# Optimization experiments

Hardware: AMD Instinct MI355X
Metric: run time of the kernel (lower is better)

The kernel has to match this reference:

```python
import jax, jax.numpy as jnp
import numpy as np

N, D, H = 4096, 1024, 16
GAMMA = 1.0


def setup_inputs() -> dict:
    key = jax.random.key(0)
    ks = jax.random.split(key, 10)
    s = 1.0 / np.sqrt(D)
    return {
        "x": jax.random.normal(ks[0], (N, D), jnp.float32),
        "h": jax.random.normal(ks[1], (N,), jnp.float32),
        "Wq": jax.random.normal(ks[2], (D, D), jnp.float32) * s,
        "bq": jax.random.normal(ks[3], (D,), jnp.float32) * s,
        "Wk": jax.random.normal(ks[4], (D, D), jnp.float32) * s,
        "bk": jax.random.normal(ks[5], (D,), jnp.float32) * s,
        "Wv": jax.random.normal(ks[6], (D, D), jnp.float32) * s,
        "bv": jax.random.normal(ks[7], (D,), jnp.float32) * s,
        "Wo": jax.random.normal(ks[8], (D, D), jnp.float32) * s,
        "bo": jax.random.normal(ks[9], (D,), jnp.float32) * s,
    }


def reference(x, h, Wq, bq, Wk, bk, Wv, bv, Wo, bo):
    n, d = x.shape
    d_head = d // H
    # torch Linear: y = x @ W.T + b
    q = (x @ Wq.T + bq).reshape(n, H, d_head)
    k = (x @ Wk.T + bk).reshape(n, H, d_head)
    v = (x @ Wv.T + bv).reshape(n, H, d_head)
    scale = 1.0 / np.sqrt(d_head).astype(np.float32)
    logits = jnp.einsum('nhd,mhd->hnm', q, k) * scale  # (H, n, n)
    logits = logits - (GAMMA * h)[None, None, :]       # per-key additive bias
    attn = jax.nn.softmax(logits, axis=-1)
    out = jnp.einsum('hnm,mhd->nhd', attn, v).reshape(n, d)
    return out @ Wo.T + bo + x
```

## Files before the change

kernel.cpp:

```cpp
#include <hip/hip_runtime.h>
#include <hip/hip_bf16.h>
#include <stdint.h>

#define NTOK 4096
#define DM   1024
#define NH   16
#define DH   64
#define SCL  0.1803368801111129f
#define LOG2E 1.4426950408889634f

typedef __attribute__((ext_vector_type(8)))  short bf16x8;
typedef __attribute__((ext_vector_type(4)))  float f32x4;
typedef __attribute__((ext_vector_type(16))) float f32x16;
typedef __attribute__((ext_vector_type(4)))  unsigned short us4;

__device__ inline unsigned short f2bf(float f) {
  union { float f; unsigned int u; } a;
  a.f = f;
  unsigned int u = a.u;
  u += 0x7fffu + ((u >> 16) & 1u);
  return (unsigned short)(u >> 16);
}

__device__ inline unsigned int cvtpk_bf16(float lo, float hi) {
  unsigned int r;
  asm("v_cvt_pk_bf16_f32 %0, %1, %2" : "=v"(r) : "v"(lo), "v"(hi));
  return r;
}

__device__ inline void gload_lds16(const void* gsrc, void* ldst) {
  __builtin_amdgcn_global_load_lds(
      (const __attribute__((address_space(1))) void*)(uintptr_t)gsrc,
      (__attribute__((address_space(3))) void*)(unsigned int)(uintptr_t)ldst,
      16, 0, 0);
}

__global__ void cvt_fused(const float* __restrict__ x,
                          const float* __restrict__ Wq,
                          const float* __restrict__ Wk,
                          const float* __restrict__ Wv,
                          const float* __restrict__ Wo,
                          const float* __restrict__ h,
                          unsigned short* __restrict__ xb,
                          unsigned short* __restrict__ wqkvb,
                          unsigned short* __restrict__ wob,
                          float* __restrict__ hperm) {
  const int b = blockIdx.x;
  if (b >= 8192) {
    int i = (b - 8192) * 256 + threadIdx.x;
    int r  = i & 15;
    int hh = (i >> 4) & 1;
    int t  = i >> 5;
    int key = t * 32 + (r & 3) + 8 * (r >> 2) + 4 * hh;
    hperm[i] = -LOG2E * h[key];
    return;
  }
  int i = b * 256 + threadIdx.x;
  const float* src; unsigned short* dst; int off;
  if (i < 1048576)      { src = x;  dst = xb;                 off = i; }
  else if (i < 1310720) { src = Wq; dst = wqkvb;              off = i - 1048576; }
  else if (i < 1572864) { src = Wk; dst = wqkvb + DM * DM;    off = i - 1310720; }
  else if (i < 1835008) { src = Wv; dst = wqkvb + 2 * DM * DM; off = i - 1572864; }
  else                  { src = Wo; dst = wob;                off = i - 1835008; }
  float4 v = ((const float4*)src)[off];
  us4 o;
  o[0] = f2bf(v.x); o[1] = f2bf(v.y); o[2] = f2bf(v.z); o[3] = f2bf(v.w);
  ((us4*)dst)[off] = o;
}

__global__ __launch_bounds__(256)
void gemm_qkv(const unsigned short* __restrict__ A,
              const unsigned short* __restrict__ B,
              const float* __restrict__ bq, const float* __restrict__ bk,
              const float* __restrict__ bv,
              unsigned short* __restrict__ Qb, unsigned short* __restrict__ Kb,
              unsigned short* __restrict__ Vt)
{
  const int bid = blockIdx.x;
  const int wg  = (bid & 7) * 96 + (bid >> 3);
  const int bn  = (wg % 24) * 128;
  const int bm  = (wg / 24) * 128;
  const int tid  = threadIdx.x;
  const int wid  = tid >> 6;
  const int lane = tid & 63;
  const int wr = wid >> 1;
  const int wc = wid & 1;

  __shared__ __align__(16) unsigned short As[128 * 32];
  __shared__ __align__(16) unsigned short Bs[128 * 32];

  f32x4 acc[4][4];
#pragma unroll
  for (int i = 0; i < 4; i++)
#pragma unroll
    for (int j = 0; j < 4; j++) acc[i][j] = f32x4{0.f, 0.f, 0.f, 0.f};

  const int fr = lane & 15;
  const int fk = (lane >> 4) * 8;
  const int srow = lane >> 2;
  const int scol = (lane & 3) * 8;

  for (int k0 = 0; k0 < DM; k0 += 32) {
#pragma unroll
    for (int c = 0; c < 2; ++c) {
      const int chunk = wid * 2 + c;
      gload_lds16(A + (size_t)(bm + chunk * 16 + srow) * DM + k0 + scol,
                  &As[chunk * 512]);
      gload_lds16(B + (size_t)(bn + chunk * 16 + srow) * DM + k0 + scol,
                  &Bs[chunk * 512]);
    }
    __syncthreads();
    bf16x8 af[4], bfr[4];
#pragma unroll
    for (int i = 0; i < 4; i++)
      af[i] = *(const bf16x8*)&As[(wr * 64 + i * 16 + fr) * 32 + fk];
#pragma unroll
    for (int j = 0; j < 4; j++)
      bfr[j] = *(const bf16x8*)&Bs[(wc * 64 + j * 16 + fr) * 32 + fk];
#pragma unroll
    for (int i = 0; i < 4; i++)
#pragma unroll
      for (int j = 0; j < 4; j++)
        acc[i][j] = __builtin_amdgcn_mfma_f32_16x16x32_bf16(af[i], bfr[j],
                                                            acc[i][j], 0, 0, 0);
    __syncthreads();
  }

  const int fq = lane >> 4;
  const int region = bn >> 10;
  const float* bias = (region == 0) ? bq : (region == 1) ? bk : bv;
  const float qscale = (region == 0) ? SCL : 1.0f;
  unsigned short* outp = (region == 0) ? Qb : Kb;
#pragma unroll
  for (int j = 0; j < 4; j++) {
    const int col = bn + wc * 64 + j * 16 + fr;
    const int cl  = col & 1023;
    const float bvx = bias[cl];
#pragma unroll
    for (int i = 0; i < 4; i++) {
      const int row0 = bm + wr * 64 + i * 16 + fq * 4;
      if (region < 2) {
#pragma unroll
        for (int r = 0; r < 4; r++)
          outp[(size_t)(row0 + r) * DM + cl] = f2bf((acc[i][j][r] + bvx) * qscale);
      } else {
        us4 pk;
#pragma unroll
        for (int r = 0; r < 4; r++) pk[r] = f2bf(acc[i][j][r] + bvx);
        *(us4*)&Vt[(size_t)cl * NTOK + row0] = pk;
      }
    }
  }
}

__global__ __launch_bounds__(256)
void gemm_out(const unsigned short* __restrict__ A,
              const unsigned short* __restrict__ B,
              const float* __restrict__ bias,
              const float* __restrict__ resid,
              float* __restrict__ Cf)
{
  const int bid = blockIdx.x;
  const int wg  = (bid & 7) * 64 + (bid >> 3);
  const int bn  = (wg % 16) * 64;
  const int bm  = (wg / 16) * 128;
  const int tid  = threadIdx.x;
  const int wid  = tid >> 6;
  const int lane = tid & 63;

  __shared__ __align__(16) unsigned short As[128 * 32];
  __shared__ __align__(16) unsigned short Bs[64 * 32];

  f32x4 acc[2][4];
#pragma unroll
  for (int i = 0; i < 2; i++)
#pragma unroll
    for (int j = 0; j < 4; j++) acc[i][j] = f32x4{0.f, 0.f, 0.f, 0.f};

  const int fr = lane & 15;
  const int fk = (lane >> 4) * 8;
  const int srow = lane >> 2;
  const int scol = (lane & 3) * 8;

  for (int k0 = 0; k0 < DM; k0 += 32) {
#pragma unroll
    for (int c = 0; c < 3; ++c) {
      const int chunk = wid * 3 + c;
      if (chunk < 8) {
        gload_lds16(A + (size_t)(bm + chunk * 16 + srow) * DM + k0 + scol,
                    &As[chunk * 512]);
      } else {
        gload_lds16(B + (size_t)(bn + (chunk - 8) * 16 + srow) * DM + k0 + scol,
                    &Bs[(chunk - 8) * 512]);
      }
    }
    __syncthreads();
    bf16x8 af[2], bfr[4];
#pragma unroll
    for (int i = 0; i < 2; i++)
      af[i] = *(const bf16x8*)&As[(wid * 32 + i * 16 + fr) * 32 + fk];
#pragma unroll
    for (int j = 0; j < 4; j++)
      bfr[j] = *(const bf16x8*)&Bs[(j * 16 + fr) * 32 + fk];
#pragma unroll
    for (int i = 0; i < 2; i++)
#pragma unroll
      for (int j = 0; j < 4; j++)
        acc[i][j] = __builtin_amdgcn_mfma_f32_16x16x32_bf16(af[i], bfr[j],
                                                            acc[i][j], 0, 0, 0);
    __syncthreads();
  }

  const int fq = lane >> 4;
#pragma unroll
  for (int j = 0; j < 4; j++) {
    const int col = bn + j * 16 + fr;
    const float bvx = bias[col];
#pragma unroll
    for (int i = 0; i < 2; i++) {
      const int row0 = bm + wid * 32 + i * 16 + fq * 4;
#pragma unroll
      for (int r = 0; r < 4; r++) {
        const size_t idx = (size_t)(row0 + r) * DM + col;
        Cf[idx] = acc[i][j][r] + bvx + resid[idx];
      }
    }
  }
}

#define MFMA32(a, b, c) __builtin_amdgcn_mfma_f32_32x32x16_bf16(a, b, c, 0, 0, 0)

__global__ __launch_bounds__(512)
void attn_kernel(const unsigned short* __restrict__ Q,
                 const unsigned short* __restrict__ K,
                 const unsigned short* __restrict__ Vt,
                 const float* __restrict__ hperm,
                 unsigned short* __restrict__ O)
{
  const int wgid = (blockIdx.x & 7) * 64 + (blockIdx.x >> 3);
  const int head = wgid >> 5;
  const int qblk = wgid & 31;
  const int tid  = threadIdx.x;
  const int wid  = tid >> 6;
  const int grp  = wid >> 2;
  const int w4   = wid & 3;
  const int lane = tid & 63;
  const int c31  = lane & 31;
  const int hi   = lane >> 5;
  const int qwb  = qblk * 128 + w4 * 32;
  const int k0g  = grp * 2048;

  __shared__ __align__(16) char lds_raw[32768];
  char* kbase = lds_raw + grp * 16384;
  char* vbase = kbase + 8192;

  const int srow = w4 * 4 + (lane >> 4);
  const int ssl  = lane & 15;
  const int kq   = ssl ^ srow;
  const int kkey = srow + 16 * (kq >> 3);
  const unsigned short* kg =
      K + (size_t)(k0g + kkey) * DM + head * DH + (kq & 7) * 8;
  const int vd = (kq >> 2) * 16 + srow;
  const unsigned short* vg =
      Vt + (size_t)(head * DH + vd) * NTOK + k0g + (kq & 3) * 8;

  const int fr15 = c31 & 15;
  const int fkh  = c31 >> 4;
  int koffB[4], voffB[2][2];
#pragma unroll
  for (int f = 0; f < 4; f++)
    koffB[f] = fr15 * 256 + (((fkh * 8 + f * 2 + hi) ^ fr15) << 4);
#pragma unroll
  for (int db = 0; db < 2; db++)
#pragma unroll
    for (int ko = 0; ko < 2; ko++)
      voffB[db][ko] =
          fr15 * 256 + ((((db * 2 + fkh) * 4 + ko * 2 + hi) ^ fr15) << 4);

  const unsigned short* qp = Q + (size_t)(qwb + c31) * DM + head * DH + hi * 8;
  const bf16x8 qf0 = *(const bf16x8*)(qp);
  const bf16x8 qf1 = *(const bf16x8*)(qp + 16);
  const bf16x8 qf2 = *(const bf16x8*)(qp + 32);
  const bf16x8 qf3 = *(const bf16x8*)(qp + 48);

  f32x16 o0, o1;
#pragma unroll
  for (int i = 0; i < 16; i++) { o0[i] = 0.f; o1[i] = 0.f; }
  float l = 0.f;

  gload_lds16(kg, kbase + w4 * 1024);
  gload_lds16(vg, vbase + w4 * 1024);
  __syncthreads();

  int cur = 0;
  const int NT = 2048 / 32;
  for (int t = 0; t < NT; ++t) {
    if (t + 1 < NT) {
      gload_lds16(kg + (size_t)(t + 1) * 32 * DM,
                  kbase + (cur ^ 1) * 4096 + w4 * 1024);
      gload_lds16(vg + (t + 1) * 32,
                  vbase + (cur ^ 1) * 4096 + w4 * 1024);
    }

    const float* hp = hperm + k0g + t * 32 + hi * 16;
    const float4 b0 = *(const float4*)(hp + 0);
    const float4 b1 = *(const float4*)(hp + 4);
    const float4 b2 = *(const float4*)(hp + 8);
    const float4 b3 = *(const float4*)(hp + 12);

    const char* Kb = kbase + cur * 4096;
    const char* Vb = vbase + cur * 4096;
    const bf16x8 kf0 = *(const bf16x8*)(Kb + koffB[0]);
    const bf16x8 kf1 = *(const bf16x8*)(Kb + koffB[1]);
    const bf16x8 kf2 = *(const bf16x8*)(Kb + koffB[2]);
    const bf16x8 kf3 = *(const bf16x8*)(Kb + koffB[3]);

    f32x16 s;
    s[0]  = b0.x; s[1]  = b0.y; s[2]  = b0.z; s[3]  = b0.w;
    s[4]  = b1.x; s[5]  = b1.y; s[6]  = b1.z; s[7]  = b1.w;
    s[8]  = b2.x; s[9]  = b2.y; s[10] = b2.z; s[11] = b2.w;
    s[12] = b3.x; s[13] = b3.y; s[14] = b3.z; s[15] = b3.w;

    s = MFMA32(kf0, qf0, s);
    s = MFMA32(kf1, qf1, s);
    s = MFMA32(kf2, qf2, s);
    s = MFMA32(kf3, qf3, s);

    const bf16x8 v00 = *(const bf16x8*)(Vb + voffB[0][0]);
    const bf16x8 v01 = *(const bf16x8*)(Vb + voffB[0][1]);
    const bf16x8 v10 = *(const bf16x8*)(Vb + voffB[1][0]);
    const bf16x8 v11 = *(const bf16x8*)(Vb + voffB[1][1]);

    float ps[16];
#pragma unroll
    for (int r = 0; r < 16; r++) ps[r] = __builtin_amdgcn_exp2f(s[r]);
    l += (((ps[0] + ps[1]) + (ps[2] + ps[3])) +
          ((ps[4] + ps[5]) + (ps[6] + ps[7]))) +
         (((ps[8] + ps[9]) + (ps[10] + ps[11])) +
          ((ps[12] + ps[13]) + (ps[14] + ps[15])));

    unsigned int X1 = cvtpk_bf16(ps[0],  ps[1]);
    unsigned int X2 = cvtpk_bf16(ps[2],  ps[3]);
    unsigned int Y1 = cvtpk_bf16(ps[4],  ps[5]);
    unsigned int Y2 = cvtpk_bf16(ps[6],  ps[7]);
    asm("v_permlane32_swap_b32 %0, %1" : "+v"(X1), "+v"(Y1));
    asm("v_permlane32_swap_b32 %0, %1" : "+v"(X2), "+v"(Y2));
    unsigned int X3 = cvtpk_bf16(ps[8],  ps[9]);
    unsigned int X4 = cvtpk_bf16(ps[10], ps[11]);
    unsigned int Y3 = cvtpk_bf16(ps[12], ps[13]);
    unsigned int Y4 = cvtpk_bf16(ps[14], ps[15]);
    asm("v_permlane32_swap_b32 %0, %1" : "+v"(X3), "+v"(Y3));
    asm("v_permlane32_swap_b32 %0, %1" : "+v"(X4), "+v"(Y4));

    union { unsigned int u[4]; bf16x8 v; } P0, P1;
    P0.u[0] = X1; P0.u[1] = X2; P0.u[2] = Y1; P0.u[3] = Y2;
    P1.u[0] = X3; P1.u[1] = X4; P1.u[2] = Y3; P1.u[3] = Y4;

    o0 = MFMA32(v00, P0.v, o0);
    o0 = MFMA32(v01, P1.v, o0);
    o1 = MFMA32(v10, P0.v, o1);
    o1 = MFMA32(v11, P1.v, o1);

    __syncthreads();
    cur ^= 1;
  }

  l += __shfl_xor(l, 32, 64);

  float* mo = (float*)lds_raw;
  float* mL = (float*)(lds_raw + 17408);
  float* row = &mo[(w4 * 64 + lane) * 17];
#pragma unroll
  for (int half = 0; half < 2; half++) {
    __syncthreads();
    if (grp == 1) {
      const f32x16& hA = half ? o1 : o0;
#pragma unroll
      for (int i = 0; i < 16; i++) row[i] = hA[i];
      if (half == 0 && hi == 0) mL[w4 * 32 + c31] = l;
    }
    __syncthreads();
    if (grp == 0) {
      f32x16& hA = half ? o1 : o0;
#pragma unroll
      for (int i = 0; i < 16; i++) hA[i] += row[i];
      if (half == 0) l += mL[w4 * 32 + c31];
    }
  }

  if (grp == 0) {
    const float inv = 1.0f / l;
    unsigned short* ob = O + (size_t)(qwb + c31) * DM + head * DH;
#pragma unroll
    for (int g = 0; g < 4; g++) {
      us4 pk;
      pk[0] = f2bf(o0[4 * g + 0] * inv); pk[1] = f2bf(o0[4 * g + 1] * inv);
      pk[2] = f2bf(o0[4 * g + 2] * inv); pk[3] = f2bf(o0[4 * g + 3] * inv);
      *(us4*)(ob + 8 * g + 4 * hi) = pk;
      pk[0] = f2bf(o1[4 * g + 0] * inv); pk[1] = f2bf(o1[4 * g + 1] * inv);
      pk[2] = f2bf(o1[4 * g + 2] * inv); pk[3] = f2bf(o1[4 * g + 3] * inv);
      *(us4*)(ob + 32 + 8 * g + 4 * hi) = pk;
    }
  }
}

extern "C" void kernel_launch(void* const* d_in, const int* in_sizes, int n_in,
                              void* d_out, int out_size, void* d_ws, size_t ws_size,
                              hipStream_t stream) {
  const float* x  = (const float*)d_in[0];
  const float* h  = (const float*)d_in[1];
  const float* Wq = (const float*)d_in[2];
  const float* bq = (const float*)d_in[3];
  const float* Wk = (const float*)d_in[4];
  const float* bk = (const float*)d_in[5];
  const float* Wv = (const float*)d_in[6];
  const float* bv = (const float*)d_in[7];
  const float* Wo = (const float*)d_in[8];
  const float* bo = (const float*)d_in[9];
  float* out = (float*)d_out;

  char* ws = (char*)d_ws;
  const size_t MB = 1 << 20;
  unsigned short* xb    = (unsigned short*)(ws + 0 * MB);
  unsigned short* wqkvb = (unsigned short*)(ws + 8 * MB);
  unsigned short* wob   = (unsigned short*)(ws + 14 * MB);
  unsigned short* Qb    = (unsigned short*)(ws + 16 * MB);
  unsigned short* Kb    = (unsigned short*)(ws + 24 * MB);
  unsigned short* Vtb   = (unsigned short*)(ws + 32 * MB);
  unsigned short* AOb   = (unsigned short*)(ws + 40 * MB);
  float*          hperm = (float*)(ws + 48 * MB);

  cvt_fused<<<8208, 256, 0, stream>>>(x, Wq, Wk, Wv, Wo, h,
                                      xb, wqkvb, wob, hperm);

  gemm_qkv<<<768, 256, 0, stream>>>(xb, wqkvb, bq, bk, bv, Qb, Kb, Vtb);

  attn_kernel<<<dim3(512), 512, 0, stream>>>(Qb, Kb, Vtb, hperm, AOb);

  gemm_out<<<512, 256, 0, stream>>>(AOb, wob, bo, x, out);
}
```

Baseline: 169.5 us.

## Split attention over key quarters with separate partial-sum reduction kernel

Replaces the single fused attention kernel (512 blocks of 512 threads, two key halves reduced in-block) with a split-K kernel that launches 2048 blocks of 256 threads, each covering a quarter of the keys and writing unnormalized fp32 partial outputs and row sums to workspace. A second kernel sums the four partials, normalizes, and writes bf16 output. The aim is more blocks to fill the GPU and fewer threads per block. The cost is roughly 64 MB of extra fp32 partial-output traffic plus an extra launch. The fused path is kept as a fallback when the workspace is too small.

```diff
diff --git a/kernel.cpp b/kernel.cpp
--- a/kernel.cpp
+++ b/kernel.cpp
@@ -230,12 +230,191 @@
 
 #define MFMA32(a, b, c) __builtin_amdgcn_mfma_f32_32x32x16_bf16(a, b, c, 0, 0, 0)
 
-__global__ __launch_bounds__(512)
-void attn_kernel(const unsigned short* __restrict__ Q,
+__global__ __launch_bounds__(256)
+void attn_splitk(const unsigned short* __restrict__ Q,
                  const unsigned short* __restrict__ K,
                  const unsigned short* __restrict__ Vt,
                  const float* __restrict__ hperm,
+                 float* __restrict__ part,
+                 float* __restrict__ lbuf)
+{
+  const int wgid = (blockIdx.x & 7) * 256 + (blockIdx.x >> 3);
+  const int head = wgid >> 7;
+  const int qblk = (wgid >> 2) & 31;
+  const int kq   = wgid & 3;
+  const int tid  = threadIdx.x;
+  const int wid  = tid >> 6;
+  const int lane = tid & 63;
+  const int c31  = lane & 31;
+  const int hi   = lane >> 5;
+  const int qwb  = qblk * 128 + wid * 32;
+  const int k0g  = kq * 1024;
+
+  __shared__ __align__(16) char lds_raw[16384];
+  char* kbase = lds_raw;
+  char* vbase = lds_raw + 8192;
+
+  const int srow = wid * 4 + (lane >> 4);
+  const int ssl  = lane & 15;
+  const int sq   = ssl ^ srow;
+  const int kkey = srow + 16 * (sq >> 3);
+  const unsigned short* kg =
+      K + (size_t)(k0g + kkey) * DM + head * DH + (sq & 7) * 8;
+  const int vd = (sq >> 2) * 16 + srow;
+  const unsigned short* vg =
+      Vt + (size_t)(head * DH + vd) * NTOK + k0g + (sq & 3) * 8;
+
+  const int fr15 = c31 & 15;
+  const int fkh  = c31 >> 4;
+  int koffB[4], voffB[2][2];
+#pragma unroll
+  for (int f = 0; f < 4; f++)
+    koffB[f] = fr15 * 256 + (((fkh * 8 + f * 2 + hi) ^ fr15) << 4);
+#pragma unroll
+  for (int db = 0; db < 2; db++)
+#pragma unroll
+    for (int ko = 0; ko < 2; ko++)
+      voffB[db][ko] =
+          fr15 * 256 + ((((db * 2 + fkh) * 4 + ko * 2 + hi) ^ fr15) << 4);
+
+  const unsigned short* qp = Q + (size_t)(qwb + c31) * DM + head * DH + hi * 8;
+  const bf16x8 qf0 = *(const bf16x8*)(qp);
+  const bf16x8 qf1 = *(const bf16x8*)(qp + 16);
+  const bf16x8 qf2 = *(const bf16x8*)(qp + 32);
+  const bf16x8 qf3 = *(const bf16x8*)(qp + 48);
+
+  f32x16 o0, o1;
+#pragma unroll
+  for (int i = 0; i < 16; i++) { o0[i] = 0.f; o1[i] = 0.f; }
+  float l = 0.f;
+
+  gload_lds16(kg, kbase + wid * 1024);
+  gload_lds16(vg, vbase + wid * 1024);
+  __syncthreads();
+
+  int cur = 0;
+  const int NT = 1024 / 32;
+  for (int t = 0; t < NT; ++t) {
+    if (t + 1 < NT) {
+      gload_lds16(kg + (size_t)(t + 1) * 32 * DM,
+                  kbase + (cur ^ 1) * 4096 + wid * 1024);
+      gload_lds16(vg + (t + 1) * 32,
+                  vbase + (cur ^ 1) * 4096 + wid * 1024);
+    }
+
+    const float* hp = hperm + k0g + t * 32 + hi * 16;
+    const float4 b0 = *(const float4*)(hp + 0);
+    const float4 b1 = *(const float4*)(hp + 4);
+    const float4 b2 = *(const float4*)(hp + 8);
+    const float4 b3 = *(const float4*)(hp + 12);
+
+    const char* Kb = kbase + cur * 4096;
+    const char* Vb = vbase + cur * 4096;
+    const bf16x8 kf0 = *(const bf16x8*)(Kb + koffB[0]);
+    const bf16x8 kf1 = *(const bf16x8*)(Kb + koffB[1]);
+    const bf16x8 kf2 = *(const bf16x8*)(Kb + koffB[2]);
+    const bf16x8 kf3 = *(const bf16x8*)(Kb + koffB[3]);
+
+    f32x16 s;
+    s[0]  = b0.x; s[1]  = b0.y; s[2]  = b0.z; s[3]  = b0.w;
+    s[4]  = b1.x; s[5]  = b1.y; s[6]  = b1.z; s[7]  = b1.w;
+    s[8]  = b2.x; s[9]  = b2.y; s[10] = b2.z; s[11] = b2.w;
+    s[12] = b3.x; s[13] = b3.y; s[14] = b3.z; s[15] = b3.w;
+
+    s = MFMA32(kf0, qf0, s);
+    s = MFMA32(kf1, qf1, s);
+    s = MFMA32(kf2, qf2, s);
+    s = MFMA32(kf3, qf3, s);
+
+    const bf16x8 v00 = *(const bf16x8*)(Vb + voffB[0][0]);
+    const bf16x8 v01 = *(const bf16x8*)(Vb + voffB[0][1]);
+    const bf16x8 v10 = *(const bf16x8*)(Vb + voffB[1][0]);
+    const bf16x8 v11 = *(const bf16x8*)(Vb + voffB[1][1]);
+
+    float ps[16];
+#pragma unroll
+    for (int r = 0; r < 16; r++) ps[r] = __builtin_amdgcn_exp2f(s[r]);
+    l += (((ps[0] + ps[1]) + (ps[2] + ps[3])) +
+          ((ps[4] + ps[5]) + (ps[6] + ps[7]))) +
+         (((ps[8] + ps[9]) + (ps[10] + ps[11])) +
+          ((ps[12] + ps[13]) + (ps[14] + ps[15])));
+
+    unsigned int X1 = cvtpk_bf16(ps[0],  ps[1]);
+    unsigned int X2 = cvtpk_bf16(ps[2],  ps[3]);
+    unsigned int Y1 = cvtpk_bf16(ps[4],  ps[5]);
+    unsigned int Y2 = cvtpk_bf16(ps[6],  ps[7]);
+    asm("v_permlane32_swap_b32 %0, %1" : "+v"(X1), "+v"(Y1));
+    asm("v_permlane32_swap_b32 %0, %1" : "+v"(X2), "+v"(Y2));
+    unsigned int X3 = cvtpk_bf16(ps[8],  ps[9]);
+    unsigned int X4 = cvtpk_bf16(ps[10], ps[11]);
+    unsigned int Y3 = cvtpk_bf16(ps[12], ps[13]);
+    unsigned int Y4 = cvtpk_bf16(ps[14], ps[15]);
+    asm("v_permlane32_swap_b32 %0, %1" : "+v"(X3), "+v"(Y3));
+    asm("v_permlane32_swap_b32 %0, %1" : "+v"(X4), "+v"(Y4));
+
+    union { unsigned int u[4]; bf16x8 v; } P0, P1;
+    P0.u[0] = X1; P0.u[1] = X2; P0.u[2] = Y1; P0.u[3] = Y2;
+    P1.u[0] = X3; P1.u[1] = X4; P1.u[2] = Y3; P1.u[3] = Y4;
+
+    o0 = MFMA32(v00, P0.v, o0);
+    o0 = MFMA32(v01, P1.v, o0);
+    o1 = MFMA32(v10, P0.v, o1);
+    o1 = MFMA32(v11, P1.v, o1);
+
+    __syncthreads();
+    cur ^= 1;
+  }
+
+  l += __shfl_xor(l, 32, 64);
+
+  float4* pb = (float4*)part + ((size_t)wgid * 4 + wid) * 8 * 64;
+#pragma unroll
+  for (int g = 0; g < 4; g++) {
+    pb[g * 64 + lane] = float4{o0[4 * g], o0[4 * g + 1], o0[4 * g + 2], o0[4 * g + 3]};
+    pb[(4 + g) * 64 + lane] = float4{o1[4 * g], o1[4 * g + 1], o1[4 * g + 2], o1[4 * g + 3]};
+  }
+  if (hi == 0) lbuf[wgid * 128 + wid * 32 + c31] = l;
+}
+
+__global__ __launch_bounds__(256)
+void attn_reduce(const float* __restrict__ part,
+                 const float* __restrict__ lbuf,
                  unsigned short* __restrict__ O)
+{
+  const int t = blockIdx.x * 256 + threadIdx.x;
+  const int lane = t & 63;
+  const int G    = (t >> 6) & 7;
+  const int wave = (t >> 9) & 3;
+  const int qblk = (t >> 11) & 31;
+  const int head = t >> 16;
+  const int c31  = lane & 31;
+  const int hi   = lane >> 5;
+
+  const int base = (head * 32 + qblk) * 4;
+  float4 s4 = float4{0.f, 0.f, 0.f, 0.f};
+  float lsum = 0.f;
+#pragma unroll
+  for (int kq = 0; kq < 4; kq++) {
+    const float4 p = ((const float4*)part)[((size_t)(base + kq) * 4 + wave) * 8 * 64
+                                           + G * 64 + lane];
+    s4.x += p.x; s4.y += p.y; s4.z += p.z; s4.w += p.w;
+    lsum += lbuf[(base + kq) * 128 + wave * 32 + c31];
+  }
+  const float inv = 1.0f / lsum;
+  const int q = qblk * 128 + wave * 32 + c31;
+  const int d = 8 * (G & 3) + 4 * hi + 32 * (G >> 2);
+  us4 pk;
+  pk[0] = f2bf(s4.x * inv); pk[1] = f2bf(s4.y * inv);
+  pk[2] = f2bf(s4.z * inv); pk[3] = f2bf(s4.w * inv);
+  *(us4*)&O[(size_t)q * DM + head * DH + d] = pk;
+}
+
+__global__ __launch_bounds__(512)
+void attn_fused(const unsigned short* __restrict__ Q,
+                const unsigned short* __restrict__ K,
+                const unsigned short* __restrict__ Vt,
+                const float* __restrict__ hperm,
+                unsigned short* __restrict__ O)
 {
   const int wgid = (blockIdx.x & 7) * 64 + (blockIdx.x >> 3);
   const int head = wgid >> 5;
@@ -256,13 +435,13 @@
 
   const int srow = w4 * 4 + (lane >> 4);
   const int ssl  = lane & 15;
-  const int kq   = ssl ^ srow;
-  const int kkey = srow + 16 * (kq >> 3);
+  const int sq   = ssl ^ srow;
+  const int kkey = srow + 16 * (sq >> 3);
   const unsigned short* kg =
-      K + (size_t)(k0g + kkey) * DM + head * DH + (kq & 7) * 8;
-  const int vd = (kq >> 2) * 16 + srow;
+      K + (size_t)(k0g + kkey) * DM + head * DH + (sq & 7) * 8;
+  const int vd = (sq >> 2) * 16 + srow;
   const unsigned short* vg =
-      Vt + (size_t)(head * DH + vd) * NTOK + k0g + (kq & 3) * 8;
+      Vt + (size_t)(head * DH + vd) * NTOK + k0g + (sq & 3) * 8;
 
   const int fr15 = c31 & 15;
   const int fkh  = c31 >> 4;
@@ -429,13 +608,20 @@
   unsigned short* Vtb   = (unsigned short*)(ws + 32 * MB);
   unsigned short* AOb   = (unsigned short*)(ws + 40 * MB);
   float*          hperm = (float*)(ws + 48 * MB);
+  float*          part  = (float*)(ws + 49 * MB);
+  float*          lbuf  = (float*)(ws + 113 * MB);
 
   cvt_fused<<<8208, 256, 0, stream>>>(x, Wq, Wk, Wv, Wo, h,
                                       xb, wqkvb, wob, hperm);
 
   gemm_qkv<<<768, 256, 0, stream>>>(xb, wqkvb, bq, bk, bv, Qb, Kb, Vtb);
 
-  attn_kernel<<<dim3(512), 512, 0, stream>>>(Qb, Kb, Vtb, hperm, AOb);
+  if (ws_size >= (size_t)115 * MB) {
+    attn_splitk<<<2048, 256, 0, stream>>>(Qb, Kb, Vtb, hperm, part, lbuf);
+    attn_reduce<<<4096, 256, 0, stream>>>(part, lbuf, AOb);
+  } else {
+    attn_fused<<<dim3(512), 512, 0, stream>>>(Qb, Kb, Vtb, hperm, AOb);
+  }
 
   gemm_out<<<512, 256, 0, stream>>>(AOb, wob, bo, x, out);
 }
```

Result: slower. 185.5 us (+9.4%).
